# Kernel tuning notes

Hardware: AMD Instinct MI355X
Metric: run time of the kernel (lower is better)

Reference implementation:

```python
import jax, jax.numpy as jnp
import numpy as np

DIM = 1024
HEADS = 16
HD = DIM // HEADS          # 64
SPECIAL = 8                # CLS/register tokens with full attention
GRID = 32                  # 32x32 patch grid
N = SPECIAL + GRID * GRID  # 1032
B = 8
WINDOW = 3                 # 2D sliding-window radius (7x7 box)
EPS = 1e-6


def _make_2d_mask() -> jnp.ndarray:
    """[N, N] bool mask: special tokens attend everywhere; patches use 2D local box."""
    idx = np.arange(N)
    special = (idx[:, None] < SPECIAL) | (idx[None, :] < SPECIAL)
    p = idx - SPECIAL
    r, c = p // GRID, p % GRID
    swa = (np.abs(r[:, None] - r[None, :]) <= WINDOW) & (np.abs(c[:, None] - c[None, :]) <= WINDOW)
    return jnp.asarray(special | swa)

_MASK = _make_2d_mask()


def setup_inputs() -> dict:
    key = jax.random.key(0)
    k1, k2, k3 = jax.random.split(key, 3)
    hidden_states = jax.random.normal(k1, (B, N, DIM), dtype=jnp.float32)
    qkv_w = jax.random.normal(k2, (3 * DIM, DIM), dtype=jnp.float32) * 0.02
    out_w = jax.random.normal(k3, (DIM, DIM), dtype=jnp.float32) * 0.02
    norm_q_w = jnp.ones((HD,), dtype=jnp.float32)
    norm_k_w = jnp.ones((HD,), dtype=jnp.float32)
    # Standard RoPE tables, half-dim frequencies tiled twice (rotate-half convention)
    pos = np.arange(N, dtype=np.float32)
    inv_freq = 1.0 / (10000.0 ** (np.arange(0, HD, 2, dtype=np.float32) / HD))
    ang = pos[:, None] * inv_freq[None, :]              # [N, HD/2]
    freqs_cos = jnp.asarray(np.concatenate([np.cos(ang), np.cos(ang)], axis=-1))  # [N, HD]
    freqs_sin = jnp.asarray(np.concatenate([np.sin(ang), np.sin(ang)], axis=-1))
    return dict(hidden_states=hidden_states, freqs_cos=freqs_cos, freqs_sin=freqs_sin,
                qkv_w=qkv_w, out_w=out_w, norm_q_w=norm_q_w, norm_k_w=norm_k_w)


def _rms_norm(x, w):
    return x * jax.lax.rsqrt(jnp.mean(x * x, axis=-1, keepdims=True) + EPS) * w


def _rotate_half(x):
    return jnp.concatenate([-x[..., HD // 2:], x[..., :HD // 2]], axis=-1)


def reference(hidden_states, freqs_cos, freqs_sin, qkv_w, out_w, norm_q_w, norm_k_w):
    Bn, Nn, C = hidden_states.shape
    # Fused QKV projection -> [3, B, H, N, D]
    qkv = (hidden_states @ qkv_w.T).reshape(Bn, Nn, 3, HEADS, HD).transpose(2, 0, 3, 1, 4)
    q, k, v = qkv[0], qkv[1], qkv[2]
    # per-head-dim RMSNorm on q, k
    q = _rms_norm(q, norm_q_w)
    k = _rms_norm(k, norm_k_w)
    # RoPE
    cos = freqs_cos[None, None]  # [1,1,N,D]
    sin = freqs_sin[None, None]
    q = q * cos + _rotate_half(q) * sin
    k = k * cos + _rotate_half(k) * sin
    # 2D sliding-window + global-token masked attention
    scale = 1.0 / jnp.sqrt(jnp.asarray(HD, dtype=q.dtype))
    scores = jnp.einsum('bhqd,bhkd->bhqk', q, k) * scale
    neg = jnp.asarray(jnp.finfo(scores.dtype).min, scores.dtype)
    scores = jnp.where(_MASK[None, None], scores, neg)
    probs = jax.nn.softmax(scores, axis=-1)
    attn = jnp.einsum('bhqk,bhkd->bhqd', probs, v)
    attn = attn.transpose(0, 2, 1, 3).reshape(Bn, Nn, C)
    return attn @ out_w.T
```

## Files before the change

### kernel.cpp

```cpp
#include <hip/hip_runtime.h>
#include <hip/hip_bf16.h>

typedef unsigned short ushort_t;
typedef __bf16 bf16x8 __attribute__((ext_vector_type(8)));
typedef float f32x4 __attribute__((ext_vector_type(4)));
typedef float f32x8 __attribute__((ext_vector_type(8)));

#define NTOK 1032
#define NROWS 8256
#define DIMC 1024
#define QKV_ELEMS 8454144
#define XE 8454144
#define QWE 3145728
#define OWE 1048576

__device__ __forceinline__ float bf2f(ushort_t u) {
    union { unsigned int i; float f; } v; v.i = ((unsigned int)u) << 16; return v.f;
}
__device__ __forceinline__ ushort_t f2bf(float f) {
    union { float f; unsigned int i; } v; v.f = f;
    unsigned int r = v.i + 0x7fffu + ((v.i >> 16) & 1u);
    return (ushort_t)(r >> 16);
}
__device__ __forceinline__ bf16x8 cvt8(const float* p) {
    const float4 a = *(const float4*)p;
    const float4 b = *(const float4*)(p + 4);
    bf16x8 r;
    r[0] = (__bf16)a.x; r[1] = (__bf16)a.y; r[2] = (__bf16)a.z; r[3] = (__bf16)a.w;
    r[4] = (__bf16)b.x; r[5] = (__bf16)b.y; r[6] = (__bf16)b.z; r[7] = (__bf16)b.w;
    return r;
}
__device__ __forceinline__ void load_lds16(const ushort_t* g, ushort_t* l) {
    __builtin_amdgcn_global_load_lds(
        (const __attribute__((address_space(1))) unsigned int*)g,
        (__attribute__((address_space(3))) unsigned int*)l, 16, 0, 0);
}

__global__ __launch_bounds__(256) void cvt_kernel(
    const float* __restrict__ X, const float* __restrict__ Wq,
    const float* __restrict__ Wo,
    ushort_t* __restrict__ Xb, ushort_t* __restrict__ Wqb,
    ushort_t* __restrict__ Wob)
{
    const long i8 = ((long)blockIdx.x * 256 + threadIdx.x) * 8;
    const float* src;
    ushort_t* dst;
    long off;
    if (i8 < XE)            { src = X;  dst = Xb;  off = i8; }
    else if (i8 < XE + QWE) { src = Wq; dst = Wqb; off = i8 - XE; }
    else                    { src = Wo; dst = Wob; off = i8 - XE - QWE; }
    *(bf16x8*)(dst + off) = cvt8(src + off);
}

template<int MODE>
__global__ __launch_bounds__(256) void gemm_kernel(
    const ushort_t* __restrict__ A, const ushort_t* __restrict__ W,
    ushort_t* __restrict__ QKV, float* __restrict__ Out)
{
    __shared__ __align__(16) ushort_t As0[128 * 32];
    __shared__ __align__(16) ushort_t As1[128 * 32];
    __shared__ __align__(16) ushort_t Bs0[128 * 32];
    __shared__ __align__(16) ushort_t Bs1[128 * 32];
    const int tid  = threadIdx.x;
    const int wave = tid >> 6, lane = tid & 63;
    const int m0 = blockIdx.y * 128;
    const int n0 = blockIdx.x * 128;
    const bool swap = (MODE == 1) || (blockIdx.x < 16);

    f32x4 acc[4][4] = {};

    const int s0 = tid, s1 = tid + 256;
    int ar0 = m0 + (s0 >> 2); if (ar0 > NROWS - 1) ar0 = NROWS - 1;
    int ar1 = m0 + (s1 >> 2); if (ar1 > NROWS - 1) ar1 = NROWS - 1;
    const int br0 = n0 + (s0 >> 2);
    const int br1 = n0 + (s1 >> 2);
    const int kc0 = (s0 & 3) * 8, kc1 = (s1 & 3) * 8;

    const ushort_t* ga0 = A + (long)ar0 * DIMC + kc0;
    const ushort_t* ga1 = A + (long)ar1 * DIMC + kc1;
    const ushort_t* gw0 = W + (long)br0 * DIMC + kc0;
    const ushort_t* gw1 = W + (long)br1 * DIMC + kc1;
    ushort_t* la00 = &As0[s0 * 8]; ushort_t* la01 = &As1[s0 * 8];
    ushort_t* la10 = &As0[s1 * 8]; ushort_t* la11 = &As1[s1 * 8];
    ushort_t* lb00 = &Bs0[s0 * 8]; ushort_t* lb01 = &Bs1[s0 * 8];
    ushort_t* lb10 = &Bs0[s1 * 8]; ushort_t* lb11 = &Bs1[s1 * 8];

    const int wm = (wave >> 1) * 64, wn = (wave & 1) * 64;
    const int fr = lane & 15, fk = (lane >> 4) * 8;
    const int arow = (wm + fr) * 32 + fk;
    const int brow = (wn + fr) * 32 + fk;

    for (int k0 = 0; k0 < DIMC; k0 += 64) {
        load_lds16(ga0 + k0,      la00);
        load_lds16(ga0 + k0 + 32, la01);
        load_lds16(ga1 + k0,      la10);
        load_lds16(ga1 + k0 + 32, la11);
        load_lds16(gw0 + k0,      lb00);
        load_lds16(gw0 + k0 + 32, lb01);
        load_lds16(gw1 + k0,      lb10);
        load_lds16(gw1 + k0 + 32, lb11);
        __syncthreads();

        {
            bf16x8 af[4], bfr[4];
            #pragma unroll
            for (int mi = 0; mi < 4; ++mi)
                af[mi] = *(const bf16x8*)&As0[arow + mi * 16 * 32];
            #pragma unroll
            for (int ni = 0; ni < 4; ++ni)
                bfr[ni] = *(const bf16x8*)&Bs0[brow + ni * 16 * 32];
            if (swap) {
                #pragma unroll
                for (int mi = 0; mi < 4; ++mi)
                    #pragma unroll
                    for (int ni = 0; ni < 4; ++ni)
                        acc[mi][ni] = __builtin_amdgcn_mfma_f32_16x16x32_bf16(
                            bfr[ni], af[mi], acc[mi][ni], 0, 0, 0);
            } else {
                #pragma unroll
                for (int mi = 0; mi < 4; ++mi)
                    #pragma unroll
                    for (int ni = 0; ni < 4; ++ni)
                        acc[mi][ni] = __builtin_amdgcn_mfma_f32_16x16x32_bf16(
                            af[mi], bfr[ni], acc[mi][ni], 0, 0, 0);
            }
        }
        {
            bf16x8 af[4], bfr[4];
            #pragma unroll
            for (int mi = 0; mi < 4; ++mi)
                af[mi] = *(const bf16x8*)&As1[arow + mi * 16 * 32];
            #pragma unroll
            for (int ni = 0; ni < 4; ++ni)
                bfr[ni] = *(const bf16x8*)&Bs1[brow + ni * 16 * 32];
            if (swap) {
                #pragma unroll
                for (int mi = 0; mi < 4; ++mi)
                    #pragma unroll
                    for (int ni = 0; ni < 4; ++ni)
                        acc[mi][ni] = __builtin_amdgcn_mfma_f32_16x16x32_bf16(
                            bfr[ni], af[mi], acc[mi][ni], 0, 0, 0);
            } else {
                #pragma unroll
                for (int mi = 0; mi < 4; ++mi)
                    #pragma unroll
                    for (int ni = 0; ni < 4; ++ni)
                        acc[mi][ni] = __builtin_amdgcn_mfma_f32_16x16x32_bf16(
                            af[mi], bfr[ni], acc[mi][ni], 0, 0, 0);
            }
        }
        __syncthreads();
    }

    const int col = lane & 15, rb = (lane >> 4) * 4;

    if (MODE == 0 && swap) {
        const int part = n0 >> 10;
        #pragma unroll
        for (int mi = 0; mi < 4; ++mi) {
            const int m = m0 + wm + mi * 16 + col;
            if (m < NROWS) {
                const int bb = m / NTOK, n = m - bb * NTOK;
                #pragma unroll
                for (int ni = 0; ni < 4; ++ni) {
                    const int rem = (n0 & 1023) + wn + ni * 16 + rb;
                    const int hg = rem >> 6, d = rem & 63;
                    ushort4 pk;
                    pk.x = f2bf(acc[mi][ni][0]);
                    pk.y = f2bf(acc[mi][ni][1]);
                    pk.z = f2bf(acc[mi][ni][2]);
                    pk.w = f2bf(acc[mi][ni][3]);
                    *(ushort4*)(QKV + (long)part * QKV_ELEMS +
                        ((long)(bb * 16 + hg) * NTOK + n) * 64 + d) = pk;
                }
            }
        }
    } else if (MODE == 0) {
        #pragma unroll
        for (int ni = 0; ni < 4; ++ni) {
            const int o = n0 + wn + ni * 16 + col;
            const int rem = o & 1023;
            const int hg = rem >> 6, d = rem & 63;
            #pragma unroll
            for (int mi = 0; mi < 4; ++mi) {
                const int mb = m0 + wm + mi * 16 + rb;
                if (mb < NROWS) {
                    const int bb = mb / NTOK, n = mb - bb * NTOK;
                    ushort4 pk;
                    pk.x = f2bf(acc[mi][ni][0]);
                    pk.y = f2bf(acc[mi][ni][1]);
                    pk.z = f2bf(acc[mi][ni][2]);
                    pk.w = f2bf(acc[mi][ni][3]);
                    *(ushort4*)(QKV + 2L * QKV_ELEMS +
                        ((long)((bb * 16 + hg) * 64 + d)) * NTOK + n) = pk;
                }
            }
        }
    } else {
        #pragma unroll
        for (int mi = 0; mi < 4; ++mi) {
            const int m = m0 + wm + mi * 16 + col;
            if (m < NROWS) {
                #pragma unroll
                for (int ni = 0; ni < 4; ++ni) {
                    const int o = n0 + wn + ni * 16 + rb;
                    float4 pk;
                    pk.x = acc[mi][ni][0];
                    pk.y = acc[mi][ni][1];
                    pk.z = acc[mi][ni][2];
                    pk.w = acc[mi][ni][3];
                    *(float4*)(Out + (long)m * DIMC + o) = pk;
                }
            }
        }
    }
}

__global__ __launch_bounds__(256) void rope_kernel(
    ushort_t* __restrict__ Qb, ushort_t* __restrict__ Kb,
    const float* __restrict__ cosb, const float* __restrict__ sinb,
    const float* __restrict__ wq, const float* __restrict__ wk)
{
    __shared__ float wsh[64];
    const int idx = blockIdx.x * 256 + threadIdx.x;
    const int tensor = (idx >= 132096) ? 1 : 0;
    const int r = idx - tensor * 132096;
    const int n = r % NTOK;
    if (threadIdx.x < 64) wsh[threadIdx.x] = (tensor ? wk : wq)[threadIdx.x];
    __syncthreads();

    ushort_t* base = (tensor ? Kb : Qb) + (long)r * 64;
    bf16x8 xc[8];
    #pragma unroll
    for (int c = 0; c < 8; ++c) xc[c] = *(const bf16x8*)(base + c * 8);

    float ss = 0.f;
    #pragma unroll
    for (int c = 0; c < 8; ++c) {
        const f32x8 xf = __builtin_convertvector(xc[c], f32x8);
        #pragma unroll
        for (int e = 0; e < 8; ++e) ss += xf[e] * xf[e];
    }
    const float rms = rsqrtf(ss * (1.0f / 64.0f) + 1e-6f);

    const float* cosp = cosb + n * 64;
    const float* sinp = sinb + n * 64;
    #pragma unroll
    for (int c = 0; c < 8; ++c) {
        const f32x8 xf = __builtin_convertvector(xc[c], f32x8);
        const f32x8 pf = __builtin_convertvector(xc[c ^ 4], f32x8);
        const float sgn = (c < 4) ? -1.f : 1.f;
        bf16x8 o8;
        #pragma unroll
        for (int e = 0; e < 8; ++e) {
            const float xn  = xf[e] * rms * wsh[c * 8 + e];
            const float rot = sgn * pf[e] * rms * wsh[(c ^ 4) * 8 + e];
            o8[e] = (__bf16)(xn * cosp[c * 8 + e] + rot * sinp[c * 8 + e]);
        }
        *(bf16x8*)(base + c * 8) = o8;
    }
}

__global__ __launch_bounds__(256) void attn_kernel(
    const ushort_t* __restrict__ Qb, const ushort_t* __restrict__ Kb,
    const ushort_t* __restrict__ Vt, ushort_t* __restrict__ AO)
{
    __shared__ __align__(16) ushort_t KP_s[256 * 72];

    const int tid = threadIdx.x;
    const int wave = tid >> 6, lane = tid & 63;
    const int m_ = lane & 15, quad = lane >> 4;
    const int nb = wave * 64;
    const int d0 = wave * 16;

    bf16x8 ones;
    #pragma unroll
    for (int e = 0; e < 8; ++e) ones[e] = (__bf16)1.0f;

    if (blockIdx.x >= 128) {
        const int blk = blockIdx.x - 128;
        const int bh = blk & 127, qr = blk >> 7;
        const int b = bh >> 4, h = bh & 15;

        int r0 = qr - 3; if (r0 < 0) r0 = 0;
        int r1 = qr + 3; if (r1 > 31) r1 = 31;
        const int limit = 8 + (r1 - r0 + 1) * 32;

        const ushort_t* Qg  = Qb + ((long)bh * NTOK + 8 + qr * 32) * 64;
        const ushort_t* Kg  = Kb + (long)bh * NTOK * 64;
        const ushort_t* Vtg = Vt + (long)bh * 64 * NTOK;

        bf16x8 af[2][2];
        #pragma unroll
        for (int mt = 0; mt < 2; ++mt)
            #pragma unroll
            for (int ks = 0; ks < 2; ++ks)
                af[mt][ks] = *(const bf16x8*)(Qg + (mt * 16 + m_) * 64 + ks * 32 + quad * 8);

        bf16x8 bv[8];
        #pragma unroll
        for (int ks = 0; ks < 8; ++ks) {
            const int slot0 = ks * 32 + quad * 8;
            int tok0;
            if (slot0 >= limit) tok0 = 0;
            else if (slot0 < 8) tok0 = slot0;
            else tok0 = 8 + r0 * 32 + (slot0 - 8);
            bv[ks] = *(const bf16x8*)(Vtg + (long)(d0 + m_) * NTOK + tok0);
        }

        for (int c = tid; c < limit * 8; c += 256) {
            const int slot = c >> 3, c8 = (c & 7) * 8;
            const int tok = slot + (slot >= 8 ? r0 * 32 : 0);
            *(bf16x8*)&KP_s[slot * 72 + c8] = *(const bf16x8*)(Kg + (long)tok * 64 + c8);
        }
        __syncthreads();

        bf16x8 bfr[4][2];
        #pragma unroll
        for (int nt = 0; nt < 4; ++nt)
            #pragma unroll
            for (int ks = 0; ks < 2; ++ks)
                bfr[nt][ks] = *(const bf16x8*)&KP_s[(nb + nt * 16 + m_) * 72 + ks * 32 + quad * 8];

        f32x4 sacc[2][4] = {};
        #pragma unroll
        for (int mt = 0; mt < 2; ++mt)
            #pragma unroll
            for (int nt = 0; nt < 4; ++nt) {
                sacc[mt][nt] = __builtin_amdgcn_mfma_f32_16x16x32_bf16(
                    af[mt][0], bfr[nt][0], sacc[mt][nt], 0, 0, 0);
                sacc[mt][nt] = __builtin_amdgcn_mfma_f32_16x16x32_bf16(
                    af[mt][1], bfr[nt][1], sacc[mt][nt], 0, 0, 0);
            }
        __syncthreads();

        #pragma unroll
        for (int mt = 0; mt < 2; ++mt)
            #pragma unroll
            for (int nt = 0; nt < 4; ++nt) {
                const int slot = nb + nt * 16 + m_;
                const int kc = (slot - 8) & 31;
                #pragma unroll
                for (int reg = 0; reg < 4; ++reg) {
                    const int qm = mt * 16 + quad * 4 + reg;
                    const bool val = (slot < 8) ||
                        ((slot < limit) && ((unsigned)(kc - qm + 3) <= 6u));
                    const float p = val ? __expf(sacc[mt][nt][reg] * 0.125f) : 0.f;
                    KP_s[qm * 280 + slot] = f2bf(p);
                }
            }
        __syncthreads();

        f32x4 oacc[2] = {}, lacc[2] = {};
        #pragma unroll
        for (int ks = 0; ks < 8; ++ks) {
            #pragma unroll
            for (int mt = 0; mt < 2; ++mt) {
                const bf16x8 ap = *(const bf16x8*)&KP_s[(mt * 16 + m_) * 280 + ks * 32 + quad * 8];
                oacc[mt] = __builtin_amdgcn_mfma_f32_16x16x32_bf16(ap, bv[ks], oacc[mt], 0, 0, 0);
                lacc[mt] = __builtin_amdgcn_mfma_f32_16x16x32_bf16(ap, ones,   lacc[mt], 0, 0, 0);
            }
        }
        #pragma unroll
        for (int mt = 0; mt < 2; ++mt)
            #pragma unroll
            for (int reg = 0; reg < 4; ++reg) {
                const int qm = mt * 16 + quad * 4 + reg;
                const int tok = 8 + qr * 32 + qm;
                AO[((long)(b * NTOK + tok)) * DIMC + h * 64 + d0 + m_] =
                    f2bf(oacc[mt][reg] / lacc[mt][reg]);
            }
    } else {
        const int bh = blockIdx.x;
        const int b = bh >> 4, h = bh & 15;
        const ushort_t* Kg  = Kb + (long)bh * NTOK * 64;
        const ushort_t* Vtg = Vt + (long)bh * 64 * NTOK;

        bf16x8 afs[2];
        if (m_ < 8) {
            #pragma unroll
            for (int ks = 0; ks < 2; ++ks)
                afs[ks] = *(const bf16x8*)(Qb + ((long)bh * NTOK + m_) * 64 + ks * 32 + quad * 8);
        } else {
            #pragma unroll
            for (int ks = 0; ks < 2; ++ks)
                #pragma unroll
                for (int e = 0; e < 8; ++e) afs[ks][e] = (__bf16)0.f;
        }

        f32x4 oacc = {}, lacc = {};
        for (int ch = 0; ch < 5; ++ch) {
            const int tok0 = ch * 256;
            const int limit = (NTOK - tok0 < 256) ? (NTOK - tok0) : 256;

            bf16x8 bv[8];
            #pragma unroll
            for (int ks = 0; ks < 8; ++ks) {
                const int slot0 = ks * 32 + quad * 8;
                const int tok = tok0 + ((slot0 < limit) ? slot0 : 0);
                bv[ks] = *(const bf16x8*)(Vtg + (long)(d0 + m_) * NTOK + tok);
            }

            __syncthreads();
            for (int c = tid; c < limit * 8; c += 256) {
                const int slot = c >> 3, c8 = (c & 7) * 8;
                *(bf16x8*)&KP_s[slot * 72 + c8] =
                    *(const bf16x8*)(Kg + (long)(tok0 + slot) * 64 + c8);
            }
            __syncthreads();

            bf16x8 bfr[4][2];
            #pragma unroll
            for (int nt = 0; nt < 4; ++nt)
                #pragma unroll
                for (int ks = 0; ks < 2; ++ks)
                    bfr[nt][ks] = *(const bf16x8*)&KP_s[(nb + nt * 16 + m_) * 72 + ks * 32 + quad * 8];
            f32x4 sacc[4] = {};
            #pragma unroll
            for (int nt = 0; nt < 4; ++nt) {
                sacc[nt] = __builtin_amdgcn_mfma_f32_16x16x32_bf16(afs[0], bfr[nt][0], sacc[nt], 0, 0, 0);
                sacc[nt] = __builtin_amdgcn_mfma_f32_16x16x32_bf16(afs[1], bfr[nt][1], sacc[nt], 0, 0, 0);
            }
            __syncthreads();

            #pragma unroll
            for (int nt = 0; nt < 4; ++nt) {
                const int slot = nb + nt * 16 + m_;
                const bool val = (slot < limit);
                #pragma unroll
                for (int reg = 0; reg < 4; ++reg) {
                    const int qm = quad * 4 + reg;
                    const float p = val ? __expf(sacc[nt][reg] * 0.125f) : 0.f;
                    KP_s[qm * 280 + slot] = f2bf(p);
                }
            }
            __syncthreads();

            #pragma unroll
            for (int ks = 0; ks < 8; ++ks) {
                const bf16x8 ap = *(const bf16x8*)&KP_s[m_ * 280 + ks * 32 + quad * 8];
                oacc = __builtin_amdgcn_mfma_f32_16x16x32_bf16(ap, bv[ks], oacc, 0, 0, 0);
                lacc = __builtin_amdgcn_mfma_f32_16x16x32_bf16(ap, ones,   lacc, 0, 0, 0);
            }
        }

        #pragma unroll
        for (int reg = 0; reg < 4; ++reg) {
            const int qm = quad * 4 + reg;
            if (qm < 8) {
                AO[((long)(b * NTOK + qm)) * DIMC + h * 64 + d0 + m_] =
                    f2bf(oacc[reg] / lacc[reg]);
            }
        }
    }
}

extern "C" void kernel_launch(void* const* d_in, const int* in_sizes, int n_in,
                              void* d_out, int out_size, void* d_ws, size_t ws_size,
                              hipStream_t stream) {
    const float* X    = (const float*)d_in[0];
    const float* fc   = (const float*)d_in[1];
    const float* fs   = (const float*)d_in[2];
    const float* qkvw = (const float*)d_in[3];
    const float* outw = (const float*)d_in[4];
    const float* nqw  = (const float*)d_in[5];
    const float* nkw  = (const float*)d_in[6];

    ushort_t* Qb  = (ushort_t*)d_ws;
    ushort_t* Kb  = Qb + QKV_ELEMS;
    ushort_t* Vt  = Kb + QKV_ELEMS;
    ushort_t* AO  = Vt + QKV_ELEMS;
    ushort_t* Xb  = AO + QKV_ELEMS;
    ushort_t* Wqb = Xb + XE;
    ushort_t* Wob = Wqb + QWE;
    float* Out = (float*)d_out;

    cvt_kernel<<<6176, 256, 0, stream>>>(X, qkvw, outw, Xb, Wqb, Wob);
    gemm_kernel<0><<<dim3(24, 65), 256, 0, stream>>>(Xb, Wqb, Qb, nullptr);
    rope_kernel<<<1032, 256, 0, stream>>>(Qb, Kb, fc, fs, nqw, nkw);
    attn_kernel<<<4224, 256, 0, stream>>>(Qb, Kb, Vt, AO);
    gemm_kernel<1><<<dim3(8, 65), 256, 0, stream>>>(AO, Wob, nullptr, Out);
}
```

Measured before the change: 305.3 us.

## Replace QKV projection GEMM with 256x256-tile, 8-wave pipelined kernel

```diff
diff --git a/kernel.cpp b/kernel.cpp
--- a/kernel.cpp
+++ b/kernel.cpp
@@ -52,6 +52,159 @@
     *(bf16x8*)(dst + off) = cvt8(src + off);
 }
 
+__global__ __launch_bounds__(512, 2) void gemm256_kernel(
+    const ushort_t* __restrict__ A, const ushort_t* __restrict__ W,
+    ushort_t* __restrict__ QKV)
+{
+    __shared__ __align__(16) ushort_t A_lds[2 * 16384];
+    __shared__ __align__(16) ushort_t B_lds[2 * 16384];
+
+    const int tid  = threadIdx.x;
+    const int wave = tid >> 6, lane = tid & 63;
+    const int wr = wave >> 2, wc = wave & 3;
+    const int fr = lane & 15, quad = lane >> 4;
+    const int m0 = blockIdx.y * 256;
+    const int n0 = blockIdx.x * 256;
+    const bool swap = (blockIdx.x < 8);
+
+    int aoff[4], boff[4];
+    #pragma unroll
+    for (int ld = 0; ld < 4; ++ld) {
+        const int s   = ld * 512 + tid;
+        const int row = s >> 3;
+        const int kc  = ((s & 7) ^ (row & 7)) * 8;
+        int ar = m0 + row; if (ar > NROWS - 1) ar = NROWS - 1;
+        aoff[ld] = ar * DIMC + kc;
+        boff[ld] = (n0 + row) * DIMC + kc;
+    }
+
+    const int ck0 = (quad ^ (fr & 7)) * 8;
+    const int ck1 = ((quad + 4) ^ (fr & 7)) * 8;
+    const int abase = (wr * 128 + fr) * 64;
+    const int bbase = (wc * 64 + fr) * 64;
+
+    f32x4 acc[8][4] = {};
+
+#define SA(ld, t, c) load_lds16(A + aoff[ld] + (t) * 64, \
+                                &A_lds[(c) * 16384 + ((ld) * 512 + tid) * 8])
+#define SB(ld, t, c) load_lds16(W + boff[ld] + (t) * 64, \
+                                &B_lds[(c) * 16384 + ((ld) * 512 + tid) * 8])
+#define WAIT_LGKM0 asm volatile("s_waitcnt lgkmcnt(0)" ::: "memory")
+#define WAIT_VM6   asm volatile("s_waitcnt vmcnt(6)"  ::: "memory")
+#define WAIT_VM0   asm volatile("s_waitcnt vmcnt(0)"  ::: "memory")
+
+    SB(0, 0, 0); SB(1, 0, 0); SB(2, 0, 0); SB(3, 0, 0);
+    SA(0, 0, 0); SA(1, 0, 0); SA(2, 0, 0); SA(3, 0, 0);
+    SB(0, 1, 1); SB(1, 1, 1); SB(2, 1, 1); SB(3, 1, 1);
+    SA(0, 1, 1); SA(2, 1, 1);
+    WAIT_VM6;
+    __builtin_amdgcn_s_barrier();
+
+    for (int t = 0; t < 16; ++t) {
+        const int c = t & 1, o = c ^ 1;
+        const int cb = c * 16384;
+        bf16x8 bfrag[4][2];
+        #pragma unroll
+        for (int p = 0; p < 4; ++p) {
+            bf16x8 af[2][2];
+            #pragma unroll
+            for (int mfi = 0; mfi < 2; ++mfi) {
+                af[mfi][0] = *(const bf16x8*)&A_lds[cb + abase + (p * 2 + mfi) * 1024 + ck0];
+                af[mfi][1] = *(const bf16x8*)&A_lds[cb + abase + (p * 2 + mfi) * 1024 + ck1];
+            }
+            if (p == 0) {
+                #pragma unroll
+                for (int nf = 0; nf < 4; ++nf) {
+                    bfrag[nf][0] = *(const bf16x8*)&B_lds[cb + bbase + nf * 1024 + ck0];
+                    bfrag[nf][1] = *(const bf16x8*)&B_lds[cb + bbase + nf * 1024 + ck1];
+                }
+                if (t + 1 < 16) { SA(1, t + 1, o); SA(3, t + 1, o); }
+            } else if (p == 1) {
+                if (t + 2 < 16) { SB(0, t + 2, c); SB(1, t + 2, c);
+                                  SB(2, t + 2, c); SB(3, t + 2, c); }
+            } else if (p == 2) {
+                if (t + 2 < 16) { SA(0, t + 2, c); SA(2, t + 2, c); }
+            }
+            WAIT_LGKM0;
+            if (p < 3) __builtin_amdgcn_s_barrier();
+            __builtin_amdgcn_s_setprio(1);
+            if (swap) {
+                #pragma unroll
+                for (int mfi = 0; mfi < 2; ++mfi)
+                    #pragma unroll
+                    for (int nf = 0; nf < 4; ++nf) {
+                        acc[p * 2 + mfi][nf] = __builtin_amdgcn_mfma_f32_16x16x32_bf16(
+                            bfrag[nf][0], af[mfi][0], acc[p * 2 + mfi][nf], 0, 0, 0);
+                        acc[p * 2 + mfi][nf] = __builtin_amdgcn_mfma_f32_16x16x32_bf16(
+                            bfrag[nf][1], af[mfi][1], acc[p * 2 + mfi][nf], 0, 0, 0);
+                    }
+            } else {
+                #pragma unroll
+                for (int mfi = 0; mfi < 2; ++mfi)
+                    #pragma unroll
+                    for (int nf = 0; nf < 4; ++nf) {
+                        acc[p * 2 + mfi][nf] = __builtin_amdgcn_mfma_f32_16x16x32_bf16(
+                            af[mfi][0], bfrag[nf][0], acc[p * 2 + mfi][nf], 0, 0, 0);
+                        acc[p * 2 + mfi][nf] = __builtin_amdgcn_mfma_f32_16x16x32_bf16(
+                            af[mfi][1], bfrag[nf][1], acc[p * 2 + mfi][nf], 0, 0, 0);
+                    }
+            }
+            __builtin_amdgcn_s_setprio(0);
+        }
+        if (t < 14)       { WAIT_VM6; __builtin_amdgcn_s_barrier(); }
+        else if (t == 14) { WAIT_VM0; __builtin_amdgcn_s_barrier(); }
+    }
+
+    const int rb = quad * 4;
+    if (swap) {
+        const int part   = n0 >> 10;
+        const int hgbase = ((n0 & 1023) + wc * 64) >> 6;
+        #pragma unroll
+        for (int mf = 0; mf < 8; ++mf) {
+            const int m = m0 + wr * 128 + mf * 16 + fr;
+            if (m < NROWS) {
+                const int bb = m / NTOK, n = m - bb * NTOK;
+                ushort_t* outb = QKV + (long)part * QKV_ELEMS +
+                    ((long)(bb * 16 + hgbase) * NTOK + n) * 64 + rb;
+                #pragma unroll
+                for (int nf = 0; nf < 4; ++nf) {
+                    ushort4 pk;
+                    pk.x = f2bf(acc[mf][nf][0]);
+                    pk.y = f2bf(acc[mf][nf][1]);
+                    pk.z = f2bf(acc[mf][nf][2]);
+                    pk.w = f2bf(acc[mf][nf][3]);
+                    *(ushort4*)(outb + nf * 16) = pk;
+                }
+            }
+        }
+    } else {
+        const int hg = ((n0 & 1023) + wc * 64) >> 6;
+        #pragma unroll
+        for (int nf = 0; nf < 4; ++nf) {
+            const int d = nf * 16 + fr;
+            #pragma unroll
+            for (int mf = 0; mf < 8; ++mf) {
+                const int mb = m0 + wr * 128 + mf * 16 + rb;
+                if (mb < NROWS) {
+                    const int bb = mb / NTOK, n = mb - bb * NTOK;
+                    ushort4 pk;
+                    pk.x = f2bf(acc[mf][nf][0]);
+                    pk.y = f2bf(acc[mf][nf][1]);
+                    pk.z = f2bf(acc[mf][nf][2]);
+                    pk.w = f2bf(acc[mf][nf][3]);
+                    *(ushort4*)(QKV + 2L * QKV_ELEMS +
+                        ((long)((bb * 16 + hg) * 64 + d)) * NTOK + n) = pk;
+                }
+            }
+        }
+    }
+#undef SA
+#undef SB
+#undef WAIT_LGKM0
+#undef WAIT_VM6
+#undef WAIT_VM0
+}
+
 template<int MODE>
 __global__ __launch_bounds__(256) void gemm_kernel(
     const ushort_t* __restrict__ A, const ushort_t* __restrict__ W,
@@ -476,7 +629,7 @@
     float* Out = (float*)d_out;
 
     cvt_kernel<<<6176, 256, 0, stream>>>(X, qkvw, outw, Xb, Wqb, Wob);
-    gemm_kernel<0><<<dim3(24, 65), 256, 0, stream>>>(Xb, Wqb, Qb, nullptr);
+    gemm256_kernel<<<dim3(12, 33), 512, 0, stream>>>(Xb, Wqb, Qb);
     rope_kernel<<<1032, 256, 0, stream>>>(Qb, Kb, fc, fs, nqw, nkw);
     attn_kernel<<<4224, 256, 0, stream>>>(Qb, Kb, Vt, AO);
     gemm_kernel<1><<<dim3(8, 65), 256, 0, stream>>>(AO, Wob, nullptr, Out);
```

New measurement: 305.2 us. About the same (-0.0%).
